# Kernel tuning notes

Hardware: AMD Instinct MI355X
Metric: run time of the kernel (lower is better)

## Reference

```python
import jax, jax.numpy as jnp
import numpy as np

N_EMB = 384
BLOCK_SIZE = 256


def setup_inputs() -> dict:
    key = jax.random.key(0)
    ks = jax.random.split(key, 6)
    B, T, H, D = 256, 256, 6, 64
    x = jax.random.normal(ks[0], (B, T, N_EMB), dtype=jnp.float32)
    wk = jax.random.normal(ks[1], (H, N_EMB, D), dtype=jnp.float32) * (N_EMB ** -0.5)
    wq = jax.random.normal(ks[2], (H, N_EMB, D), dtype=jnp.float32) * (N_EMB ** -0.5)
    wv = jax.random.normal(ks[3], (H, N_EMB, D), dtype=jnp.float32) * (N_EMB ** -0.5)
    wproj = jax.random.normal(ks[4], (N_EMB, N_EMB), dtype=jnp.float32) * (N_EMB ** -0.5)
    bproj = jnp.zeros((N_EMB,), dtype=jnp.float32)
    return {"x": x, "wk": wk, "wq": wq, "wv": wv, "wproj": wproj, "bproj": bproj}


def reference(x, wk, wq, wv, wproj, bproj):
    B, T, C = x.shape  # C == N_EMB
    # per-head projections (no bias), heads stacked on leading axis
    k = jnp.einsum('btc,hcd->bhtd', x, wk)
    q = jnp.einsum('btc,hcd->bhtd', x, wq)
    v = jnp.einsum('btc,hcd->bhtd', x, wv)
    # faithful to source: wei = k @ q^T scaled by sqrt(C) (embed dim, not head dim)
    wei = jnp.einsum('bhtd,bhsd->bhts', k, q) / (C ** 0.5)
    causal = jnp.tril(jnp.ones((T, T), dtype=bool))
    wei = jnp.where(causal, wei, -jnp.inf)
    wei = jax.nn.softmax(wei, axis=-1)
    # dropout is identity in eval mode
    out = jnp.einsum('bhts,bhsd->bhtd', wei, v)  # [B,H,T,D]
    out = out.transpose(0, 2, 1, 3).reshape(B, T, C)  # concat heads
    out = out @ wproj + bproj
    return out
```

## Files before the change

kernel.cpp:

```cpp
#include <hip/hip_runtime.h>

typedef unsigned short u16;
typedef __bf16 bf16x8 __attribute__((ext_vector_type(8)));
typedef float f32x4 __attribute__((ext_vector_type(4)));

#define B_SZ 256
#define T_SZ 256
#define C_EMB 384
#define NHEAD 6
#define DHEAD 64
#define N3 1152
#define BHTD 25165824
#define SCALE 0.05103103630798287f
#define MASKV -3.0e4f

__device__ __forceinline__ u16 f2bf(float f) {
  __bf16 b = (__bf16)f;
  return __builtin_bit_cast(u16, b);
}

__device__ __forceinline__ void gload_lds16(const void* g, void* l) {
  __builtin_amdgcn_global_load_lds((const __attribute__((address_space(1))) void*)g,
                                   (__attribute__((address_space(3))) void*)l, 16, 0, 0);
}

__global__ __launch_bounds__(256) void prep_all(
    const float* __restrict__ x, const float* __restrict__ wk,
    const float* __restrict__ wq, const float* __restrict__ wv,
    const float* __restrict__ wproj,
    u16* __restrict__ xb, u16* __restrict__ wqkvt, u16* __restrict__ wprojt) {
  int bidx = blockIdx.x;
  if (bidx < 12288) {
    int i = bidx * 256 + threadIdx.x;
    float4 f0 = ((const float4*)x)[i * 2];
    float4 f1 = ((const float4*)x)[i * 2 + 1];
    uint4 p;
    p.x = (unsigned)f2bf(f0.x) | ((unsigned)f2bf(f0.y) << 16);
    p.y = (unsigned)f2bf(f0.z) | ((unsigned)f2bf(f0.w) << 16);
    p.z = (unsigned)f2bf(f1.x) | ((unsigned)f2bf(f1.y) << 16);
    p.w = (unsigned)f2bf(f1.z) | ((unsigned)f2bf(f1.w) << 16);
    ((uint4*)xb)[i] = p;
  } else {
    int i = (bidx - 12288) * 256 + threadIdx.x;
    if (i < N3 * C_EMB) {
      int n = i / C_EMB, c = i - n * C_EMB;
      int tensor = n >= 768 ? 2 : (n >= 384 ? 1 : 0);
      int r = n - tensor * 384;
      int h = r >> 6, d = r & 63;
      const float* w = tensor == 0 ? wk : (tensor == 1 ? wq : wv);
      float val = w[(h * C_EMB + c) * DHEAD + d];
      if (tensor == 0) val *= SCALE;
      wqkvt[i] = f2bf(val);
    } else {
      int ii = i - N3 * C_EMB;
      if (ii < C_EMB * C_EMB) {
        int n = ii / C_EMB, c = ii - n * C_EMB;
        wprojt[ii] = f2bf(wproj[c * C_EMB + n]);
      }
    }
  }
}

__global__ __launch_bounds__(256, 4) void qkv_gemm(const u16* __restrict__ xb,
                                                   const u16* __restrict__ wt,
                                                   u16* __restrict__ kqv) {
  __shared__ __align__(16) u16 lA[128 * 64];
  __shared__ __align__(16) u16 lB[128 * 64];
  const int tid = threadIdx.x;
  const int lane = tid & 63, w = tid >> 6;
  int bid = blockIdx.x;
  int nb = (bid & 7) * 576 + (bid >> 3);
  int mt = nb / 9, nt = nb - mt * 9;
  const int n0 = nt * 128, m0 = mt * 128;
  const int wr = w >> 1, wc = w & 1;
  f32x4 acc[4][4] = {};
  for (int kt = 0; kt < 6; ++kt) {
    const int k0 = kt * 64;
#pragma unroll
    for (int it = 0; it < 4; ++it) {
      int ub = it * 256 + w * 64;
      int u = ub + lane;
      int row = u >> 3, cu = u & 7;
      int koff = k0 + ((cu ^ (row & 7)) << 3);
      gload_lds16(xb + (size_t)(m0 + row) * C_EMB + koff, lA + ub * 8);
      gload_lds16(wt + (size_t)(n0 + row) * C_EMB + koff, lB + ub * 8);
    }
    asm volatile("s_waitcnt vmcnt(0)" ::: "memory");
    asm volatile("s_barrier" ::: "memory");
    bf16x8 af[4][2], bfr[4][2];
#pragma unroll
    for (int mi = 0; mi < 4; ++mi) {
      int row = wr * 64 + mi * 16 + (lane & 15);
#pragma unroll
      for (int kk = 0; kk < 2; ++kk) {
        int cu = kk * 4 + (lane >> 4);
        af[mi][kk] = *(const bf16x8*)((const char*)lA + row * 128 + ((cu ^ (row & 7)) << 4));
      }
    }
#pragma unroll
    for (int ni = 0; ni < 4; ++ni) {
      int row = wc * 64 + ni * 16 + (lane & 15);
#pragma unroll
      for (int kk = 0; kk < 2; ++kk) {
        int cu = kk * 4 + (lane >> 4);
        bfr[ni][kk] = *(const bf16x8*)((const char*)lB + row * 128 + ((cu ^ (row & 7)) << 4));
      }
    }
#pragma unroll
    for (int kk = 0; kk < 2; ++kk)
#pragma unroll
      for (int mi = 0; mi < 4; ++mi)
#pragma unroll
        for (int ni = 0; ni < 4; ++ni)
          acc[mi][ni] = __builtin_amdgcn_mfma_f32_16x16x32_bf16(
              af[mi][kk], bfr[ni][kk], acc[mi][ni], 0, 0, 0);
    asm volatile("s_barrier" ::: "memory");
  }

  const int tensor = nt / 3;
  if (tensor == 2) {
    u16* vt = kqv + 2 * (size_t)BHTD;
#pragma unroll
    for (int ni = 0; ni < 4; ++ni) {
      int r2 = n0 + wc * 64 + ni * 16 + (lane & 15) - 768;
      int h = r2 >> 6, d = r2 & 63;
#pragma unroll
      for (int mi = 0; mi < 4; ++mi) {
        int gm0 = m0 + wr * 64 + mi * 16 + ((lane >> 4) << 2);
        int b = gm0 >> 8, tt2 = gm0 & 255;
        ushort4 pk;
        pk.x = f2bf(acc[mi][ni][0]);
        pk.y = f2bf(acc[mi][ni][1]);
        pk.z = f2bf(acc[mi][ni][2]);
        pk.w = f2bf(acc[mi][ni][3]);
        *(ushort4*)(vt + ((size_t)(b * NHEAD + h) * 64 + d) * 256 + tt2) = pk;
      }
    }
  } else {
#pragma unroll
    for (int ni = 0; ni < 4; ++ni) {
      int gn = n0 + wc * 64 + ni * 16 + (lane & 15);
      int r2 = gn - tensor * 384;
      int h = r2 >> 6, d = r2 & 63;
#pragma unroll
      for (int mi = 0; mi < 4; ++mi) {
        int gm0 = m0 + wr * 64 + mi * 16 + ((lane >> 4) << 2);
#pragma unroll
        for (int r = 0; r < 4; ++r) {
          int m = gm0 + r;
          int b = m >> 8, t = m & 255;
          kqv[(size_t)tensor * BHTD + ((((b * NHEAD + h) << 8) + t) << 6) + d] =
              f2bf(acc[mi][ni][r]);
        }
      }
    }
  }
}

__global__ __launch_bounds__(512, 2) void attn_kernel(const u16* __restrict__ kqv,
                                                      u16* __restrict__ attnb) {
  __shared__ __align__(16) u16 lQ[256 * 64];
  __shared__ __align__(16) u16 lVt[64 * 256];
  __shared__ __align__(16) char lP[8 * 16 * 128];
  const int tid = threadIdx.x;
  const int lane = tid & 63, w = tid >> 6;
  int bid = blockIdx.x;
  int id = (bid & 7) * 384 + (bid >> 3);
  const int bh = id >> 1, tt = id & 1;
  const int t0 = tt * 128;
  const u16* Kb = kqv + (size_t)bh * (T_SZ * DHEAD);
  const u16* Qb = kqv + (size_t)BHTD + (size_t)bh * (T_SZ * DHEAD);
  const u16* Vb = kqv + 2 * (size_t)BHTD + (size_t)bh * (DHEAD * T_SZ);

  const int t0w = t0 + w * 16;
  const int tg0 = t0w + ((lane >> 4) << 2);

  bf16x8 af[2];
  {
    const u16* kr = Kb + (size_t)(t0w + (lane & 15)) * DHEAD;
    af[0] = *(const bf16x8*)(kr + ((lane >> 4) << 3));
    af[1] = *(const bf16x8*)(kr + 32 + ((lane >> 4) << 3));
  }
  asm volatile("" ::: "memory");
#pragma unroll
  for (int it = 0; it < 4; ++it) {
    int u = it * 512 + tid;
    int row = u >> 3, cu = u & 7;
    gload_lds16(Qb + (size_t)row * DHEAD + ((cu ^ (row & 7)) << 3), lQ + u * 8);
  }
  asm volatile("" ::: "memory");
#pragma unroll
  for (int it = 0; it < 4; ++it) {
    int u = it * 512 + tid;
    int row = u >> 5, cu = u & 31;
    gload_lds16(Vb + (size_t)row * T_SZ + ((cu >> 3) << 6) + (((cu & 7) ^ (row & 7)) << 3),
                lVt + u * 8);
  }
  asm volatile("s_waitcnt vmcnt(4)" ::: "memory");
  asm volatile("s_barrier" ::: "memory");

  char* lPw = lP + w * (16 * 128);
  f32x4 oacc[4] = {};
  float lrowp[4] = {0.f, 0.f, 0.f, 0.f};
  const int last = t0w >> 6;

#define QK_TILE(s0_) { \
    f32x4 sacc[4] = {}; \
    __builtin_amdgcn_s_setprio(1); \
    _Pragma("unroll") for (int ni = 0; ni < 4; ++ni) { \
      int row = (s0_) + ni * 16 + (lane & 15); \
      _Pragma("unroll") for (int kk = 0; kk < 2; ++kk) { \
        int cu = kk * 4 + (lane >> 4); \
        bf16x8 bq = *(const bf16x8*)((const char*)lQ + row * 128 + ((cu ^ (row & 7)) << 4)); \
        sacc[ni] = __builtin_amdgcn_mfma_f32_16x16x32_bf16(af[kk], bq, sacc[ni], 0, 0, 0); \
      } \
    } \
    __builtin_amdgcn_s_setprio(0); \
    if ((s0_) + 63 > t0w) { \
      _Pragma("unroll") for (int ni = 0; ni < 4; ++ni) { \
        int sg = (s0_) + ni * 16 + (lane & 15); \
        _Pragma("unroll") for (int r = 0; r < 4; ++r) \
          if (sg > tg0 + r) sacc[ni][r] = MASKV; \
      } \
    } \
    _Pragma("unroll") for (int ni = 0; ni < 4; ++ni) { \
      int scol = ni * 16 + (lane & 15); \
      _Pragma("unroll") for (int r = 0; r < 4; ++r) { \
        float p = __expf(sacc[ni][r]); \
        lrowp[r] += p; \
        int trow = ((lane >> 4) << 2) + r; \
        *(u16*)(lPw + trow * 128 + ((scol * 2) ^ ((trow & 7) << 4))) = f2bf(p); \
      } \
    } }

#define PV_TILE(s0_) { \
    bf16x8 pa[2]; \
    int trow = lane & 15; \
    _Pragma("unroll") for (int kk = 0; kk < 2; ++kk) { \
      int cu = kk * 4 + (lane >> 4); \
      pa[kk] = *(const bf16x8*)(lPw + trow * 128 + (((cu) << 4) ^ ((trow & 7) << 4))); \
    } \
    __builtin_amdgcn_s_setprio(1); \
    _Pragma("unroll") for (int nd = 0; nd < 4; ++nd) { \
      int drow = nd * 16 + (lane & 15); \
      _Pragma("unroll") for (int kk = 0; kk < 2; ++kk) { \
        int cu = kk * 4 + (lane >> 4); \
        bf16x8 vb = *(const bf16x8*)((const char*)lVt + drow * 512 + (s0_) * 2 + \
                                     (((cu) ^ (drow & 7)) << 4)); \
        oacc[nd] = __builtin_amdgcn_mfma_f32_16x16x32_bf16(pa[kk], vb, oacc[nd], 0, 0, 0); \
      } \
    } \
    __builtin_amdgcn_s_setprio(0); }

  QK_TILE(0)
  asm volatile("s_waitcnt vmcnt(0)" ::: "memory");
  asm volatile("s_barrier" ::: "memory");
  PV_TILE(0)
  for (int si = 1; si <= last; ++si) {
    const int s0 = si << 6;
    QK_TILE(s0)
    PV_TILE(s0)
  }
#undef QK_TILE
#undef PV_TILE

#pragma unroll
  for (int r = 0; r < 4; ++r) {
#pragma unroll
    for (int off = 1; off < 16; off <<= 1)
      lrowp[r] += __shfl_xor(lrowp[r], off);
  }
  const int b = bh / NHEAD, h = bh - (bh / NHEAD) * NHEAD;
#pragma unroll
  for (int r = 0; r < 4; ++r) {
    int t = tg0 + r;
    float inv = 1.0f / lrowp[r];
#pragma unroll
    for (int nd = 0; nd < 4; ++nd) {
      int col = h * 64 + nd * 16 + (lane & 15);
      attnb[((size_t)(b * T_SZ + t)) * C_EMB + col] = f2bf(oacc[nd][r] * inv);
    }
  }
}

__global__ __launch_bounds__(256, 4) void out_gemm(const u16* __restrict__ a,
                                                   const u16* __restrict__ wt,
                                                   const float* __restrict__ bias,
                                                   float* __restrict__ out) {
  __shared__ __align__(16) u16 lA[128 * 64];
  __shared__ __align__(16) u16 lB[128 * 64];
  const int tid = threadIdx.x;
  const int lane = tid & 63, w = tid >> 6;
  int bid = blockIdx.x;
  int nb = (bid & 7) * 192 + (bid >> 3);
  int mt = nb / 3, nt = nb - mt * 3;
  const int n0 = nt * 128, m0 = mt * 128;
  const int wr = w >> 1, wc = w & 1;
  f32x4 acc[4][4] = {};
  for (int kt = 0; kt < 6; ++kt) {
    const int k0 = kt * 64;
#pragma unroll
    for (int it = 0; it < 4; ++it) {
      int ub = it * 256 + w * 64;
      int u = ub + lane;
      int row = u >> 3, cu = u & 7;
      int koff = k0 + ((cu ^ (row & 7)) << 3);
      gload_lds16(a + (size_t)(m0 + row) * C_EMB + koff, lA + ub * 8);
      gload_lds16(wt + (size_t)(n0 + row) * C_EMB + koff, lB + ub * 8);
    }
    asm volatile("s_waitcnt vmcnt(0)" ::: "memory");
    asm volatile("s_barrier" ::: "memory");
    bf16x8 af[4][2], bfr[4][2];
#pragma unroll
    for (int mi = 0; mi < 4; ++mi) {
      int row = wr * 64 + mi * 16 + (lane & 15);
#pragma unroll
      for (int kk = 0; kk < 2; ++kk) {
        int cu = kk * 4 + (lane >> 4);
        af[mi][kk] = *(const bf16x8*)((const char*)lA + row * 128 + ((cu ^ (row & 7)) << 4));
      }
    }
#pragma unroll
    for (int ni = 0; ni < 4; ++ni) {
      int row = wc * 64 + ni * 16 + (lane & 15);
#pragma unroll
      for (int kk = 0; kk < 2; ++kk) {
        int cu = kk * 4 + (lane >> 4);
        bfr[ni][kk] = *(const bf16x8*)((const char*)lB + row * 128 + ((cu ^ (row & 7)) << 4));
      }
    }
#pragma unroll
    for (int kk = 0; kk < 2; ++kk)
#pragma unroll
      for (int mi = 0; mi < 4; ++mi)
#pragma unroll
        for (int ni = 0; ni < 4; ++ni)
          acc[mi][ni] = __builtin_amdgcn_mfma_f32_16x16x32_bf16(
              af[mi][kk], bfr[ni][kk], acc[mi][ni], 0, 0, 0);
    asm volatile("s_barrier" ::: "memory");
  }
#pragma unroll
  for (int ni = 0; ni < 4; ++ni) {
    int gn = n0 + wc * 64 + ni * 16 + (lane & 15);
    float bv = bias[gn];
#pragma unroll
    for (int mi = 0; mi < 4; ++mi) {
      int gm0 = m0 + wr * 64 + mi * 16 + ((lane >> 4) << 2);
#pragma unroll
      for (int r = 0; r < 4; ++r)
        out[(size_t)(gm0 + r) * C_EMB + gn] = acc[mi][ni][r] + bv;
    }
  }
}

extern "C" void kernel_launch(void* const* d_in, const int* in_sizes, int n_in,
                              void* d_out, int out_size, void* d_ws, size_t ws_size,
                              hipStream_t stream) {
  const float* x = (const float*)d_in[0];
  const float* wk = (const float*)d_in[1];
  const float* wq = (const float*)d_in[2];
  const float* wv = (const float*)d_in[3];
  const float* wproj = (const float*)d_in[4];
  const float* bproj = (const float*)d_in[5];
  float* out = (float*)d_out;
  u16* ws = (u16*)d_ws;
  u16* kqv = ws;
  u16* attnb = ws + 3 * (size_t)BHTD;
  u16* xb = attnb;
  u16* wqkvt = attnb + (size_t)BHTD;
  u16* wprojt = wqkvt + (size_t)N3 * C_EMB;
  prep_all<<<14592, 256, 0, stream>>>(x, wk, wq, wv, wproj, xb, wqkvt, wprojt);
  qkv_gemm<<<4608, 256, 0, stream>>>(xb, wqkvt, kqv);
  attn_kernel<<<3072, 512, 0, stream>>>(kqv, attnb);
  out_gemm<<<1536, 256, 0, stream>>>(attnb, wprojt, bproj, out);
}
```

Before: 182.5 us.

## Process both query halves per attention block to reuse loaded Q/V tiles

Measured after the change: 179.7 us. Within noise of the previous version (-1.6%).

```diff
diff --git a/kernel.cpp b/kernel.cpp
--- a/kernel.cpp
+++ b/kernel.cpp
@@ -165,21 +165,24 @@
   const int tid = threadIdx.x;
   const int lane = tid & 63, w = tid >> 6;
   int bid = blockIdx.x;
-  int id = (bid & 7) * 384 + (bid >> 3);
-  const int bh = id >> 1, tt = id & 1;
-  const int t0 = tt * 128;
+  const int bh = (bid & 7) * 192 + (bid >> 3);
   const u16* Kb = kqv + (size_t)bh * (T_SZ * DHEAD);
   const u16* Qb = kqv + (size_t)BHTD + (size_t)bh * (T_SZ * DHEAD);
   const u16* Vb = kqv + 2 * (size_t)BHTD + (size_t)bh * (DHEAD * T_SZ);
 
-  const int t0w = t0 + w * 16;
-  const int tg0 = t0w + ((lane >> 4) << 2);
-
-  bf16x8 af[2];
+  const int t0w0 = w * 16;
+  const int t0w1 = 128 + w * 16;
+  const int tg00 = t0w0 + ((lane >> 4) << 2);
+  const int tg01 = t0w1 + ((lane >> 4) << 2);
+
+  bf16x8 af0[2], af1[2];
   {
-    const u16* kr = Kb + (size_t)(t0w + (lane & 15)) * DHEAD;
-    af[0] = *(const bf16x8*)(kr + ((lane >> 4) << 3));
-    af[1] = *(const bf16x8*)(kr + 32 + ((lane >> 4) << 3));
+    const u16* kr0 = Kb + (size_t)(t0w0 + (lane & 15)) * DHEAD;
+    const u16* kr1 = Kb + (size_t)(t0w1 + (lane & 15)) * DHEAD;
+    af0[0] = *(const bf16x8*)(kr0 + ((lane >> 4) << 3));
+    af0[1] = *(const bf16x8*)(kr0 + 32 + ((lane >> 4) << 3));
+    af1[0] = *(const bf16x8*)(kr1 + ((lane >> 4) << 3));
+    af1[1] = *(const bf16x8*)(kr1 + 32 + ((lane >> 4) << 3));
   }
   asm volatile("" ::: "memory");
 #pragma unroll
@@ -200,11 +203,13 @@
   asm volatile("s_barrier" ::: "memory");
 
   char* lPw = lP + w * (16 * 128);
-  f32x4 oacc[4] = {};
-  float lrowp[4] = {0.f, 0.f, 0.f, 0.f};
-  const int last = t0w >> 6;
-
-#define QK_TILE(s0_) { \
+  f32x4 oacc0[4] = {}, oacc1[4] = {};
+  float lrowp0[4] = {0.f, 0.f, 0.f, 0.f};
+  float lrowp1[4] = {0.f, 0.f, 0.f, 0.f};
+  const int last0 = t0w0 >> 6;
+  const int last1 = t0w1 >> 6;
+
+#define QK_TILE(s0_, af_, t0w_, tg0_) { \
     f32x4 sacc[4] = {}; \
     __builtin_amdgcn_s_setprio(1); \
     _Pragma("unroll") for (int ni = 0; ni < 4; ++ni) { \
@@ -212,28 +217,28 @@
       _Pragma("unroll") for (int kk = 0; kk < 2; ++kk) { \
         int cu = kk * 4 + (lane >> 4); \
         bf16x8 bq = *(const bf16x8*)((const char*)lQ + row * 128 + ((cu ^ (row & 7)) << 4)); \
-        sacc[ni] = __builtin_amdgcn_mfma_f32_16x16x32_bf16(af[kk], bq, sacc[ni], 0, 0, 0); \
+        sacc[ni] = __builtin_amdgcn_mfma_f32_16x16x32_bf16(af_[kk], bq, sacc[ni], 0, 0, 0); \
       } \
     } \
     __builtin_amdgcn_s_setprio(0); \
-    if ((s0_) + 63 > t0w) { \
+    if ((s0_) + 63 > (t0w_)) { \
       _Pragma("unroll") for (int ni = 0; ni < 4; ++ni) { \
         int sg = (s0_) + ni * 16 + (lane & 15); \
         _Pragma("unroll") for (int r = 0; r < 4; ++r) \
-          if (sg > tg0 + r) sacc[ni][r] = MASKV; \
+          if (sg > (tg0_) + r) sacc[ni][r] = MASKV; \
       } \
     } \
     _Pragma("unroll") for (int ni = 0; ni < 4; ++ni) { \
       int scol = ni * 16 + (lane & 15); \
       _Pragma("unroll") for (int r = 0; r < 4; ++r) { \
         float p = __expf(sacc[ni][r]); \
-        lrowp[r] += p; \
+        lrp[r] += p; \
         int trow = ((lane >> 4) << 2) + r; \
         *(u16*)(lPw + trow * 128 + ((scol * 2) ^ ((trow & 7) << 4))) = f2bf(p); \
       } \
     } }
 
-#define PV_TILE(s0_) { \
+#define PV_TILE(s0_, oacc_) { \
     bf16x8 pa[2]; \
     int trow = lane & 15; \
     _Pragma("unroll") for (int kk = 0; kk < 2; ++kk) { \
@@ -247,19 +252,33 @@
         int cu = kk * 4 + (lane >> 4); \
         bf16x8 vb = *(const bf16x8*)((const char*)lVt + drow * 512 + (s0_) * 2 + \
                                      (((cu) ^ (drow & 7)) << 4)); \
-        oacc[nd] = __builtin_amdgcn_mfma_f32_16x16x32_bf16(pa[kk], vb, oacc[nd], 0, 0, 0); \
+        oacc_[nd] = __builtin_amdgcn_mfma_f32_16x16x32_bf16(pa[kk], vb, oacc_[nd], 0, 0, 0); \
       } \
     } \
     __builtin_amdgcn_s_setprio(0); }
 
-  QK_TILE(0)
+  {
+    float* lrp = lrowp0;
+    QK_TILE(0, af0, t0w0, tg00)
+  }
   asm volatile("s_waitcnt vmcnt(0)" ::: "memory");
   asm volatile("s_barrier" ::: "memory");
-  PV_TILE(0)
-  for (int si = 1; si <= last; ++si) {
-    const int s0 = si << 6;
-    QK_TILE(s0)
-    PV_TILE(s0)
+  PV_TILE(0, oacc0)
+  {
+    float* lrp = lrowp0;
+    for (int si = 1; si <= last0; ++si) {
+      const int s0 = si << 6;
+      QK_TILE(s0, af0, t0w0, tg00)
+      PV_TILE(s0, oacc0)
+    }
+  }
+  {
+    float* lrp = lrowp1;
+    for (int si = 0; si <= last1; ++si) {
+      const int s0 = si << 6;
+      QK_TILE(s0, af1, t0w1, tg01)
+      PV_TILE(s0, oacc1)
+    }
   }
 #undef QK_TILE
 #undef PV_TILE
@@ -267,18 +286,22 @@
 #pragma unroll
   for (int r = 0; r < 4; ++r) {
 #pragma unroll
-    for (int off = 1; off < 16; off <<= 1)
-      lrowp[r] += __shfl_xor(lrowp[r], off);
+    for (int off = 1; off < 16; off <<= 1) {
+      lrowp0[r] += __shfl_xor(lrowp0[r], off);
+      lrowp1[r] += __shfl_xor(lrowp1[r], off);
+    }
   }
   const int b = bh / NHEAD, h = bh - (bh / NHEAD) * NHEAD;
 #pragma unroll
   for (int r = 0; r < 4; ++r) {
-    int t = tg0 + r;
-    float inv = 1.0f / lrowp[r];
+    int t0_ = tg00 + r, t1_ = tg01 + r;
+    float inv0 = 1.0f / lrowp0[r];
+    float inv1 = 1.0f / lrowp1[r];
 #pragma unroll
     for (int nd = 0; nd < 4; ++nd) {
       int col = h * 64 + nd * 16 + (lane & 15);
-      attnb[((size_t)(b * T_SZ + t)) * C_EMB + col] = f2bf(oacc[nd][r] * inv);
+      attnb[((size_t)(b * T_SZ + t0_)) * C_EMB + col] = f2bf(oacc0[nd][r] * inv0);
+      attnb[((size_t)(b * T_SZ + t1_)) * C_EMB + col] = f2bf(oacc1[nd][r] * inv1);
     }
   }
 }
@@ -371,6 +394,6 @@
   u16* wprojt = wqkvt + (size_t)N3 * C_EMB;
   prep_all<<<14592, 256, 0, stream>>>(x, wk, wq, wv, wproj, xb, wqkvt, wprojt);
   qkv_gemm<<<4608, 256, 0, stream>>>(xb, wqkvt, kqv);
-  attn_kernel<<<3072, 512, 0, stream>>>(kqv, attnb);
+  attn_kernel<<<1536, 512, 0, stream>>>(kqv, attnb);
   out_gemm<<<1536, 256, 0, stream>>>(attnb, wprojt, bproj, out);
 }
```
